# Kernel optimization log

Measured on AMD Instinct MI355X. Metric: run time of the kernel, lower is better.

Reference implementation:

```python
import jax, jax.numpy as jnp
import numpy as np

BATCH, IN, OUT, P = 8192, 1024, 1024, 8

def setup_inputs() -> dict:
    key = jax.random.key(0)
    k1, k2, k3 = jax.random.split(key, 3)
    x = jax.random.normal(k1, (BATCH, IN), dtype=jnp.float32)
    # per-(output,input) basis coefficients, init ~ randn*0.1 as in torch module
    coefficients = jax.random.normal(k2, (OUT, IN, P), dtype=jnp.float32) * 0.1
    weights = jax.random.normal(k3, (OUT, IN), dtype=jnp.float32)
    return {"x": x, "coefficients": coefficients, "weights": weights}

def reference(x, coefficients, weights):
    # out[b,o] = sum_i x[b,i] * (sum_p coef[o,i,p]) * weights[o,i]
    # == x @ (coef_sum * weights)^T  -- single fused GEMM
    w_eff = coefficients.sum(axis=-1) * weights  # [O, I]
    return jnp.einsum('bi,oi->bo', x, w_eff)
```

## Files before the change

### kernel.cpp

```cpp
#include <hip/hip_runtime.h>
#include <hip/hip_bf16.h>
#include <stdint.h>

#define BATCH 8192
#define IN    1024
#define OUTD  1024
#define PBASIS 8

typedef __attribute__((ext_vector_type(8))) short bf16x8;
typedef __attribute__((ext_vector_type(4))) float floatx4;

__device__ __forceinline__ unsigned short f2bf(float f) {
    union { float f; unsigned u; } v; v.f = f;
    unsigned u = v.u;
    u += 0x7fffu + ((u >> 16) & 1u);
    return (unsigned short)(u >> 16);
}

__global__ void prep_kernel(const float* __restrict__ x,
                            const float* __restrict__ coef,
                            const float* __restrict__ w,
                            unsigned short* __restrict__ xb,
                            unsigned short* __restrict__ weff) {
    int b = blockIdx.x;
    int tid = threadIdx.x;
    if (b < 4096) {
        int idx = b * 256 + tid;
        const float4* p = (const float4*)(x + (size_t)idx * 8);
        float4 a = p[0], c = p[1];
        uint4 o;
        o.x = (unsigned)f2bf(a.x) | ((unsigned)f2bf(a.y) << 16);
        o.y = (unsigned)f2bf(a.z) | ((unsigned)f2bf(a.w) << 16);
        o.z = (unsigned)f2bf(c.x) | ((unsigned)f2bf(c.y) << 16);
        o.w = (unsigned)f2bf(c.z) | ((unsigned)f2bf(c.w) << 16);
        ((uint4*)xb)[idx] = o;
    } else {
        int idx = (b - 4096) * 256 + tid;
        size_t e0 = (size_t)idx * 2;
        const float4* c4 = (const float4*)(coef + e0 * PBASIS);
        float4 a = c4[0], bb = c4[1], c = c4[2], d = c4[3];
        float s0 = (a.x + a.y + a.z + a.w) + (bb.x + bb.y + bb.z + bb.w);
        float s1 = (c.x + c.y + c.z + c.w) + (d.x + d.y + d.z + d.w);
        float2 ww = ((const float2*)w)[idx];
        unsigned b0 = f2bf(s0 * ww.x);
        unsigned b1 = f2bf(s1 * ww.y);
        ((unsigned*)weff)[idx] = b0 | (b1 << 16);
    }
}

__device__ __forceinline__ void gload_lds16(const void* g, void* l) {
    __builtin_amdgcn_global_load_lds(
        (const __attribute__((address_space(1))) unsigned int*)g,
        (__attribute__((address_space(3))) unsigned int*)l,
        16, 0, 0);
}

#define BARRIER()  asm volatile("s_barrier" ::: "memory")
#define WAIT_V6L0() asm volatile("s_waitcnt vmcnt(6) lgkmcnt(0)" ::: "memory")
#define WAIT_V0L0() asm volatile("s_waitcnt vmcnt(0) lgkmcnt(0)" ::: "memory")

__global__ __launch_bounds__(256, 2) void gemm_bt(
        const unsigned short* __restrict__ A,
        const unsigned short* __restrict__ B,
        float* __restrict__ C) {
    constexpr int K = IN, BK = 64, NT = K / BK;
    constexpr int STG = 24576;
    constexpr int ES = 68;
    __shared__ __align__(16) char smem[3 * STG];
    float* ebuf = (float*)smem;

    const int tid  = threadIdx.x;
    const int bm   = blockIdx.x, bn = blockIdx.y;
    const int lane = tid & 63;
    const int wave = tid >> 6;
    const int wm   = wave >> 1;
    const int wn   = wave & 1;
    const int t    = lane & 15;
    const int q    = lane >> 4;
    const int r8   = t & 7;

    int g0 = tid,        ra0 = g0 >> 3, ca0 = (g0 & 7) ^ (ra0 & 7);
    int g1 = 256 + tid,  ra1 = g1 >> 3, ca1 = (g1 & 7) ^ (ra1 & 7);
    int g2 = 512 + tid,  ra2 = g2 >> 3, ca2 = (g2 & 7) ^ (ra2 & 7);
    int g3 = 768 + tid,  ra3 = g3 >> 3, ca3 = (g3 & 7) ^ (ra3 & 7);
    int h0 = tid,        rb0 = h0 >> 3, cb0 = (h0 & 7) ^ (rb0 & 7);
    int h1 = 256 + tid,  rb1 = h1 >> 3, cb1 = (h1 & 7) ^ (rb1 & 7);

    const unsigned short* gA0 = A + (size_t)(bm * 128 + ra0) * K + ca0 * 8;
    const unsigned short* gA1 = A + (size_t)(bm * 128 + ra1) * K + ca1 * 8;
    const unsigned short* gA2 = A + (size_t)(bm * 128 + ra2) * K + ca2 * 8;
    const unsigned short* gA3 = A + (size_t)(bm * 128 + ra3) * K + ca3 * 8;
    const unsigned short* gB0 = B + (size_t)(bn * 64 + rb0) * K + cb0 * 8;
    const unsigned short* gB1 = B + (size_t)(bn * 64 + rb1) * K + cb1 * 8;

    const int dA0 = g0 * 16, dA1 = g1 * 16, dA2 = g2 * 16, dA3 = g3 * 16;
    const int dB0 = 16384 + h0 * 16, dB1 = 16384 + h1 * 16;

    const int aO0 = ((wm * 64 + t) * 64 + ((0 + q) ^ r8) * 8) * 2;
    const int aO1 = ((wm * 64 + t) * 64 + ((4 + q) ^ r8) * 8) * 2;
    const int bO0 = 16384 + ((wn * 32 + t) * 64 + ((0 + q) ^ r8) * 8) * 2;
    const int bO1 = 16384 + ((wn * 32 + t) * 64 + ((4 + q) ^ r8) * 8) * 2;

    floatx4 acc[4][2];
#pragma unroll
    for (int i = 0; i < 4; ++i)
#pragma unroll
        for (int j = 0; j < 2; ++j)
            acc[i][j] = (floatx4){0.f, 0.f, 0.f, 0.f};

#define STAGE_P(sp, ko)                                             \
    {                                                               \
        gload_lds16(gA0 + (ko), (sp) + dA0);                        \
        gload_lds16(gA1 + (ko), (sp) + dA1);                        \
        gload_lds16(gA2 + (ko), (sp) + dA2);                        \
    }
#define STAGE_Q(sp, ko)                                             \
    {                                                               \
        gload_lds16(gA3 + (ko), (sp) + dA3);                        \
        gload_lds16(gB0 + (ko), (sp) + dB0);                        \
        gload_lds16(gB1 + (ko), (sp) + dB1);                        \
    }
#define PHASE(sb, aO, bO)                                           \
    {                                                               \
        const char* ab = (const char*)(sb) + (aO);                  \
        const char* bb = (const char*)(sb) + (bO);                  \
        bf16x8 a0 = *(const bf16x8*)(ab + 0 * 2048);                \
        bf16x8 a1 = *(const bf16x8*)(ab + 1 * 2048);                \
        bf16x8 a2 = *(const bf16x8*)(ab + 2 * 2048);                \
        bf16x8 a3 = *(const bf16x8*)(ab + 3 * 2048);                \
        bf16x8 b0 = *(const bf16x8*)(bb + 0 * 2048);                \
        bf16x8 b1 = *(const bf16x8*)(bb + 1 * 2048);                \
        bf16x8 av[4] = {a0, a1, a2, a3};                            \
        bf16x8 bv[2] = {b0, b1};                                    \
        __builtin_amdgcn_s_setprio(1);                              \
        _Pragma("unroll")                                           \
        for (int i = 0; i < 4; ++i)                                 \
            _Pragma("unroll")                                       \
            for (int j = 0; j < 2; ++j)                             \
                acc[i][j] = __builtin_amdgcn_mfma_f32_16x16x32_bf16(\
                    av[i], bv[j], acc[i][j], 0, 0, 0);              \
        __builtin_amdgcn_s_setprio(0);                              \
    }

    {
        char* s0 = smem;
        char* s1 = smem + STG;
        STAGE_P(s0, 0); STAGE_Q(s0, 0);
        STAGE_P(s1, BK); STAGE_Q(s1, BK);
        WAIT_V6L0();
        BARRIER();
    }

    int cur = 0;
    for (int kt = 0; kt < NT; ++kt) {
        char* sb = smem + cur * STG;
        int nx = cur + 2; if (nx >= 3) nx -= 3;
        char* sp = smem + nx * STG;
        const int kpre = (kt + 2) * BK;
        const bool pre = (kt < NT - 2);

        if (pre) STAGE_P(sp, kpre);
        PHASE(sb, aO0, bO0);
        if (pre) STAGE_Q(sp, kpre);
        PHASE(sb, aO1, bO1);

        if (pre) { WAIT_V6L0(); }
        else     { WAIT_V0L0(); }
        BARRIER();
        ++cur; if (cur == 3) cur = 0;
    }
#undef PHASE
#undef STAGE_P
#undef STAGE_Q

    __syncthreads();

#pragma unroll
    for (int tm = 0; tm < 4; ++tm)
#pragma unroll
        for (int tn = 0; tn < 2; ++tn)
#pragma unroll
            for (int r = 0; r < 4; ++r)
                ebuf[(wm * 64 + tm * 16 + q * 4 + r) * ES
                     + wn * 32 + tn * 16 + t] = acc[tm][tn][r];
    __syncthreads();
#pragma unroll
    for (int ps = 0; ps < 8; ++ps) {
        int row  = ps * 16 + (tid >> 4);
        int col4 = tid & 15;
        float4 v = *(const float4*)(ebuf + row * ES + col4 * 4);
        *(float4*)(C + (size_t)(bm * 128 + row) * OUTD + bn * 64 + col4 * 4) = v;
    }
}

extern "C" void kernel_launch(void* const* d_in, const int* in_sizes, int n_in,
                              void* d_out, int out_size, void* d_ws, size_t ws_size,
                              hipStream_t stream) {
    const float* x    = (const float*)d_in[0];
    const float* coef = (const float*)d_in[1];
    const float* w    = (const float*)d_in[2];
    float* out = (float*)d_out;

    unsigned short* xb   = (unsigned short*)d_ws;
    unsigned short* weff = (unsigned short*)((char*)d_ws + (size_t)BATCH * IN * 2);

    prep_kernel<<<6144, 256, 0, stream>>>(x, coef, w, xb, weff);
    gemm_bt<<<dim3(BATCH / 128, OUTD / 64), 256, 0, stream>>>(xb, weff, out);
}
```

Baseline: 125.6 us.

## Fuse fp32-to-bf16 conversion of x into GEMM and enlarge tile to 128x128

Drops the separate pass that converts x to bf16. The GEMM now streams fp32 x tiles into LDS and converts them with packed cvt instructions just before the MFMA calls. The block tile widens to 128x128 with 512 threads and one block per CU, so each x row tile is read half as many times. In exchange the A-tile LDS traffic doubles, conversion ALU work sits inside the main loop, and 144KB of LDS per block removes any chance of co-residency.

```diff
diff --git a/kernel.cpp b/kernel.cpp
--- a/kernel.cpp
+++ b/kernel.cpp
@@ -17,35 +17,34 @@
     return (unsigned short)(u >> 16);
 }
 
-__global__ void prep_kernel(const float* __restrict__ x,
-                            const float* __restrict__ coef,
+__device__ __forceinline__ unsigned cvtpk(float lo, float hi) {
+    unsigned r;
+    asm("v_cvt_pk_bf16_f32 %0, %1, %2" : "=v"(r) : "v"(lo), "v"(hi));
+    return r;
+}
+
+__device__ __forceinline__ bf16x8 mkbf8(float4 lo, float4 hi) {
+    union { uint4 u; bf16x8 b; } x;
+    x.u.x = cvtpk(lo.x, lo.y);
+    x.u.y = cvtpk(lo.z, lo.w);
+    x.u.z = cvtpk(hi.x, hi.y);
+    x.u.w = cvtpk(hi.z, hi.w);
+    return x.b;
+}
+
+__global__ void prep_kernel(const float* __restrict__ coef,
                             const float* __restrict__ w,
-                            unsigned short* __restrict__ xb,
                             unsigned short* __restrict__ weff) {
-    int b = blockIdx.x;
-    int tid = threadIdx.x;
-    if (b < 4096) {
-        int idx = b * 256 + tid;
-        const float4* p = (const float4*)(x + (size_t)idx * 8);
-        float4 a = p[0], c = p[1];
-        uint4 o;
-        o.x = (unsigned)f2bf(a.x) | ((unsigned)f2bf(a.y) << 16);
-        o.y = (unsigned)f2bf(a.z) | ((unsigned)f2bf(a.w) << 16);
-        o.z = (unsigned)f2bf(c.x) | ((unsigned)f2bf(c.y) << 16);
-        o.w = (unsigned)f2bf(c.z) | ((unsigned)f2bf(c.w) << 16);
-        ((uint4*)xb)[idx] = o;
-    } else {
-        int idx = (b - 4096) * 256 + tid;
-        size_t e0 = (size_t)idx * 2;
-        const float4* c4 = (const float4*)(coef + e0 * PBASIS);
-        float4 a = c4[0], bb = c4[1], c = c4[2], d = c4[3];
-        float s0 = (a.x + a.y + a.z + a.w) + (bb.x + bb.y + bb.z + bb.w);
-        float s1 = (c.x + c.y + c.z + c.w) + (d.x + d.y + d.z + d.w);
-        float2 ww = ((const float2*)w)[idx];
-        unsigned b0 = f2bf(s0 * ww.x);
-        unsigned b1 = f2bf(s1 * ww.y);
-        ((unsigned*)weff)[idx] = b0 | (b1 << 16);
-    }
+    int idx = blockIdx.x * 256 + threadIdx.x;
+    size_t e0 = (size_t)idx * 2;
+    const float4* c4 = (const float4*)(coef + e0 * PBASIS);
+    float4 a = c4[0], bb = c4[1], c = c4[2], d = c4[3];
+    float s0 = (a.x + a.y + a.z + a.w) + (bb.x + bb.y + bb.z + bb.w);
+    float s1 = (c.x + c.y + c.z + c.w) + (d.x + d.y + d.z + d.w);
+    float2 ww = ((const float2*)w)[idx];
+    unsigned b0 = f2bf(s0 * ww.x);
+    unsigned b1 = f2bf(s1 * ww.y);
+    ((unsigned*)weff)[idx] = b0 | (b1 << 16);
 }
 
 __device__ __forceinline__ void gload_lds16(const void* g, void* l) {
@@ -55,17 +54,17 @@
         16, 0, 0);
 }
 
-#define BARRIER()  asm volatile("s_barrier" ::: "memory")
+#define BARRIER()   asm volatile("s_barrier" ::: "memory")
 #define WAIT_V6L0() asm volatile("s_waitcnt vmcnt(6) lgkmcnt(0)" ::: "memory")
 #define WAIT_V0L0() asm volatile("s_waitcnt vmcnt(0) lgkmcnt(0)" ::: "memory")
 
-__global__ __launch_bounds__(256, 2) void gemm_bt(
-        const unsigned short* __restrict__ A,
+__global__ __launch_bounds__(512, 1) void gemm_bt(
+        const float* __restrict__ X,
         const unsigned short* __restrict__ B,
         float* __restrict__ C) {
     constexpr int K = IN, BK = 64, NT = K / BK;
-    constexpr int STG = 24576;
-    constexpr int ES = 68;
+    constexpr int STG = 49152;
+    constexpr int ES = 132;
     __shared__ __align__(16) char smem[3 * STG];
     float* ebuf = (float*)smem;
 
@@ -73,33 +72,36 @@
     const int bm   = blockIdx.x, bn = blockIdx.y;
     const int lane = tid & 63;
     const int wave = tid >> 6;
-    const int wm   = wave >> 1;
-    const int wn   = wave & 1;
+    const int wm   = wave >> 2;
+    const int wn   = wave & 3;
     const int t    = lane & 15;
     const int q    = lane >> 4;
     const int r8   = t & 7;
 
-    int g0 = tid,        ra0 = g0 >> 3, ca0 = (g0 & 7) ^ (ra0 & 7);
-    int g1 = 256 + tid,  ra1 = g1 >> 3, ca1 = (g1 & 7) ^ (ra1 & 7);
-    int g2 = 512 + tid,  ra2 = g2 >> 3, ca2 = (g2 & 7) ^ (ra2 & 7);
-    int g3 = 768 + tid,  ra3 = g3 >> 3, ca3 = (g3 & 7) ^ (ra3 & 7);
-    int h0 = tid,        rb0 = h0 >> 3, cb0 = (h0 & 7) ^ (rb0 & 7);
-    int h1 = 256 + tid,  rb1 = h1 >> 3, cb1 = (h1 & 7) ^ (rb1 & 7);
-
-    const unsigned short* gA0 = A + (size_t)(bm * 128 + ra0) * K + ca0 * 8;
-    const unsigned short* gA1 = A + (size_t)(bm * 128 + ra1) * K + ca1 * 8;
-    const unsigned short* gA2 = A + (size_t)(bm * 128 + ra2) * K + ca2 * 8;
-    const unsigned short* gA3 = A + (size_t)(bm * 128 + ra3) * K + ca3 * 8;
-    const unsigned short* gB0 = B + (size_t)(bn * 64 + rb0) * K + cb0 * 8;
-    const unsigned short* gB1 = B + (size_t)(bn * 64 + rb1) * K + cb1 * 8;
+    int g0 = tid,         ar0 = g0 >> 4, ac0 = ((g0 & 15) ^ (ar0 & 15)) * 4;
+    int g1 = 512 + tid,   ar1 = g1 >> 4, ac1 = ((g1 & 15) ^ (ar1 & 15)) * 4;
+    int g2 = 1024 + tid,  ar2 = g2 >> 4, ac2 = ((g2 & 15) ^ (ar2 & 15)) * 4;
+    int g3 = 1536 + tid,  ar3 = g3 >> 4, ac3 = ((g3 & 15) ^ (ar3 & 15)) * 4;
+    int h0 = tid,         br0 = h0 >> 3, bc0 = ((h0 & 7) ^ (br0 & 7)) * 8;
+    int h1 = 512 + tid,   br1 = h1 >> 3, bc1 = ((h1 & 7) ^ (br1 & 7)) * 8;
+
+    const float* gx0 = X + (size_t)(bm * 128 + ar0) * K + ac0;
+    const float* gx1 = X + (size_t)(bm * 128 + ar1) * K + ac1;
+    const float* gx2 = X + (size_t)(bm * 128 + ar2) * K + ac2;
+    const float* gx3 = X + (size_t)(bm * 128 + ar3) * K + ac3;
+    const unsigned short* gB0 = B + (size_t)(bn * 128 + br0) * K + bc0;
+    const unsigned short* gB1 = B + (size_t)(bn * 128 + br1) * K + bc1;
 
     const int dA0 = g0 * 16, dA1 = g1 * 16, dA2 = g2 * 16, dA3 = g3 * 16;
-    const int dB0 = 16384 + h0 * 16, dB1 = 16384 + h1 * 16;
-
-    const int aO0 = ((wm * 64 + t) * 64 + ((0 + q) ^ r8) * 8) * 2;
-    const int aO1 = ((wm * 64 + t) * 64 + ((4 + q) ^ r8) * 8) * 2;
-    const int bO0 = 16384 + ((wn * 32 + t) * 64 + ((0 + q) ^ r8) * 8) * 2;
-    const int bO1 = 16384 + ((wn * 32 + t) * 64 + ((4 + q) ^ r8) * 8) * 2;
+    const int dB0 = 32768 + h0 * 16, dB1 = 32768 + h1 * 16;
+
+    const int aRow = (wm * 64 + t) * 256;
+    const int aL0 = aRow + (((0 + 2 * q) ^ t) * 16);
+    const int aH0 = aRow + (((1 + 2 * q) ^ t) * 16);
+    const int aL1 = aRow + (((8 + 2 * q) ^ t) * 16);
+    const int aH1 = aRow + (((9 + 2 * q) ^ t) * 16);
+    const int bO0 = 32768 + ((wn * 32 + t) * 64 + ((0 + q) ^ r8) * 8) * 2;
+    const int bO1 = 32768 + ((wn * 32 + t) * 64 + ((4 + q) ^ r8) * 8) * 2;
 
     floatx4 acc[4][2];
 #pragma unroll
@@ -110,27 +112,31 @@
 
 #define STAGE_P(sp, ko)                                             \
     {                                                               \
-        gload_lds16(gA0 + (ko), (sp) + dA0);                        \
-        gload_lds16(gA1 + (ko), (sp) + dA1);                        \
-        gload_lds16(gA2 + (ko), (sp) + dA2);                        \
+        gload_lds16(gx0 + (ko), (sp) + dA0);                        \
+        gload_lds16(gx1 + (ko), (sp) + dA1);                        \
+        gload_lds16(gx2 + (ko), (sp) + dA2);                        \
     }
 #define STAGE_Q(sp, ko)                                             \
     {                                                               \
-        gload_lds16(gA3 + (ko), (sp) + dA3);                        \
+        gload_lds16(gx3 + (ko), (sp) + dA3);                        \
         gload_lds16(gB0 + (ko), (sp) + dB0);                        \
         gload_lds16(gB1 + (ko), (sp) + dB1);                        \
     }
-#define PHASE(sb, aO, bO)                                           \
+#define PHASE(sb, aL, aH, bO)                                       \
     {                                                               \
-        const char* ab = (const char*)(sb) + (aO);                  \
-        const char* bb = (const char*)(sb) + (bO);                  \
-        bf16x8 a0 = *(const bf16x8*)(ab + 0 * 2048);                \
-        bf16x8 a1 = *(const bf16x8*)(ab + 1 * 2048);                \
-        bf16x8 a2 = *(const bf16x8*)(ab + 2 * 2048);                \
-        bf16x8 a3 = *(const bf16x8*)(ab + 3 * 2048);                \
-        bf16x8 b0 = *(const bf16x8*)(bb + 0 * 2048);                \
-        bf16x8 b1 = *(const bf16x8*)(bb + 1 * 2048);                \
-        bf16x8 av[4] = {a0, a1, a2, a3};                            \
+        const char* base = (const char*)(sb);                       \
+        float4 l0 = *(const float4*)(base + (aL) + 0 * 4096);       \
+        float4 h0_ = *(const float4*)(base + (aH) + 0 * 4096);      \
+        float4 l1 = *(const float4*)(base + (aL) + 1 * 4096);       \
+        float4 h1_ = *(const float4*)(base + (aH) + 1 * 4096);      \
+        float4 l2 = *(const float4*)(base + (aL) + 2 * 4096);       \
+        float4 h2_ = *(const float4*)(base + (aH) + 2 * 4096);      \
+        float4 l3 = *(const float4*)(base + (aL) + 3 * 4096);       \
+        float4 h3_ = *(const float4*)(base + (aH) + 3 * 4096);      \
+        bf16x8 b0 = *(const bf16x8*)(base + (bO) + 0 * 2048);       \
+        bf16x8 b1 = *(const bf16x8*)(base + (bO) + 1 * 2048);       \
+        bf16x8 av[4] = {mkbf8(l0, h0_), mkbf8(l1, h1_),             \
+                        mkbf8(l2, h2_), mkbf8(l3, h3_)};            \
         bf16x8 bv[2] = {b0, b1};                                    \
         __builtin_amdgcn_s_setprio(1);                              \
         _Pragma("unroll")                                           \
@@ -160,9 +166,9 @@
         const bool pre = (kt < NT - 2);
 
         if (pre) STAGE_P(sp, kpre);
-        PHASE(sb, aO0, bO0);
+        PHASE(sb, aL0, aH0, bO0);
         if (pre) STAGE_Q(sp, kpre);
-        PHASE(sb, aO1, bO1);
+        PHASE(sb, aL1, aH1, bO1);
 
         if (pre) { WAIT_V6L0(); }
         else     { WAIT_V0L0(); }
@@ -186,10 +192,10 @@
     __syncthreads();
 #pragma unroll
     for (int ps = 0; ps < 8; ++ps) {
-        int row  = ps * 16 + (tid >> 4);
-        int col4 = tid & 15;
+        int row  = ps * 16 + (tid >> 5);
+        int col4 = tid & 31;
         float4 v = *(const float4*)(ebuf + row * ES + col4 * 4);
-        *(float4*)(C + (size_t)(bm * 128 + row) * OUTD + bn * 64 + col4 * 4) = v;
+        *(float4*)(C + (size_t)(bm * 128 + row) * OUTD + bn * 128 + col4 * 4) = v;
     }
 }
 
@@ -201,9 +207,8 @@
     const float* w    = (const float*)d_in[2];
     float* out = (float*)d_out;
 
-    unsigned short* xb   = (unsigned short*)d_ws;
-    unsigned short* weff = (unsigned short*)((char*)d_ws + (size_t)BATCH * IN * 2);
-
-    prep_kernel<<<6144, 256, 0, stream>>>(x, coef, w, xb, weff);
-    gemm_bt<<<dim3(BATCH / 128, OUTD / 64), 256, 0, stream>>>(xb, weff, out);
-}
+    unsigned short* weff = (unsigned short*)d_ws;
+
+    prep_kernel<<<2048, 256, 0, stream>>>(coef, w, weff);
+    gemm_bt<<<dim3(BATCH / 128, OUTD / 128), 512, 0, stream>>>(x, weff, out);
+}
```

After: 152.1 us. 1.21x slower.
